# Performance work log

Measured on AMD Instinct MI355X. Metric: run time of the kernel, lower is better.

## Reference

```python
import jax, jax.numpy as jnp
import numpy as np

H = 8  # num_heads (init kwarg)

def setup_inputs() -> dict:
    key = jax.random.key(0)
    k1, k2, k3, k4 = jax.random.split(key, 4)
    B, S, E = 4, 2048, 512
    x = jax.random.normal(k1, (B, S, E), dtype=jnp.float32)
    # 'normal' keras initializer ~ N(0, 0.05)
    Wq = jax.random.normal(k2, (E, E), dtype=jnp.float32) * 0.05
    Wk = jax.random.normal(k3, (E, E), dtype=jnp.float32) * 0.05
    Wv = jax.random.normal(k4, (E, E), dtype=jnp.float32) * 0.05
    return {"x": x, "Wq": Wq, "Wk": Wk, "Wv": Wv}

def _split_heads(t):
    # [B,S,E] -> [H,B,S,E/H]; matches tf.stack(tf.split(t, H, axis=2))
    B, S, E = t.shape
    return t.reshape(B, S, H, E // H).transpose(2, 0, 1, 3)

def reference(x, Wq, Wk, Wv):
    B, S, E = x.shape
    q = _split_heads(jnp.einsum('bse,ef->bsf', x, Wq))  # [H,B,S,dh]
    k = _split_heads(jnp.einsum('bse,ef->bsf', x, Wk))
    v = _split_heads(jnp.einsum('bse,ef->bsf', x, Wv))
    # NOTE: original has NO 1/sqrt(d) scaling
    scores = jnp.einsum('hbqd,hbkd->hbqk', q, k)         # [H,B,S,S]
    attn = jax.nn.softmax(scores, axis=-1)
    effect = jnp.einsum('hbqk,hbkd->hbqd', attn, v)      # [H,B,S,dh]
    # tf.concat(tf.split(effect, H), axis=-1) + squeeze == merge heads on last dim
    out = effect.transpose(1, 2, 0, 3).reshape(B, S, E)  # [B,S,E]
    return (out, x)
```

## Files before the change

### kernel.cpp

```cpp
#include <hip/hip_runtime.h>

typedef _Float16 f16x8 __attribute__((ext_vector_type(8)));
typedef __fp16 h16x2 __attribute__((ext_vector_type(2)));
typedef float f32x4 __attribute__((ext_vector_type(4)));
typedef float f32x16 __attribute__((ext_vector_type(16)));

#define GF(r) ((((r)&3)) ^ (((r)>>2)&3))
#define LOG2E 1.44269504088896f

#define GLD16(gp, lp) __builtin_amdgcn_global_load_lds( \
    (const __attribute__((address_space(1))) void*)(gp), \
    (__attribute__((address_space(3))) void*)(lp), 16, 0, 0)

__global__ void cvt_all_kernel(const float4* __restrict__ x4, f16x8* __restrict__ xh,
                               float4* __restrict__ xc,
                               const float* __restrict__ Wq, const float* __restrict__ Wk,
                               const float* __restrict__ Wv, _Float16* __restrict__ wt) {
    const int blk = blockIdx.x;
    if (blk < 2048) {
        int i = blk * 256 + threadIdx.x;
        float4 a = x4[2 * i], b = x4[2 * i + 1];
        xc[2 * i] = a;
        xc[2 * i + 1] = b;
        f16x8 h;
        h[0] = (_Float16)a.x; h[1] = (_Float16)a.y; h[2] = (_Float16)a.z; h[3] = (_Float16)a.w;
        h[4] = (_Float16)b.x; h[5] = (_Float16)b.y; h[6] = (_Float16)b.z; h[7] = (_Float16)b.w;
        xh[i] = h;
    } else {
        int j = (blk - 2048) * 256 + threadIdx.x;
        int mat = j >> 18;
        int r = (j >> 9) & 511;
        int n = j & 511;
        const float* W = (mat == 0) ? Wq : ((mat == 1) ? Wk : Wv);
        float v = W[r * 512 + n];
        wt[(size_t)mat * 262144 + (size_t)n * 512 + r] = (_Float16)v;
    }
}

__global__ __launch_bounds__(256, 2) void gemm_qkv(
    const _Float16* __restrict__ xh, const _Float16* __restrict__ wt,
    _Float16* __restrict__ qh, _Float16* __restrict__ kh, _Float16* __restrict__ vt) {
    __shared__ __align__(16) char gsm[49152];
    const int mat = blockIdx.y;
    const _Float16* wp = wt + (size_t)mat * 262144;
    const int mtile = blockIdx.x >> 2, ntile = blockIdx.x & 3;
    const int tid = threadIdx.x, lane = tid & 63;
    const int g = lane >> 4, c = lane & 15;
    const int wid = tid >> 6, wm = wid >> 1, wn = wid & 1;

    f32x4 acc[4][4];
#pragma unroll
    for (int i = 0; i < 4; ++i)
#pragma unroll
        for (int j = 0; j < 4; ++j) acc[i][j] = (f32x4){0.f, 0.f, 0.f, 0.f};

    const int row0 = tid >> 2, p0 = tid & 3;

    auto GSTAGE = [&](int buf, int ks) {
        _Float16* la_ = (_Float16*)(gsm + buf * 16384);
        _Float16* lb_ = (_Float16*)(gsm + buf * 16384 + 8192);
        int r = row0, pp = p0 ^ GF(r);
        GLD16(xh + (size_t)(mtile * 128 + r) * 512 + ks * 32 + pp * 8, &la_[tid * 8]);
        GLD16(wp + (size_t)(ntile * 128 + r) * 512 + ks * 32 + pp * 8, &lb_[tid * 8]);
        r = 64 + row0; pp = p0 ^ GF(r);
        GLD16(xh + (size_t)(mtile * 128 + r) * 512 + ks * 32 + pp * 8, &la_[(256 + tid) * 8]);
        GLD16(wp + (size_t)(ntile * 128 + r) * 512 + ks * 32 + pp * 8, &lb_[(256 + tid) * 8]);
    };

    auto GTILE = [&](int ks) {
        const _Float16* la = (const _Float16*)(gsm + (ks % 3) * 16384);
        const _Float16* lb = (const _Float16*)(gsm + (ks % 3) * 16384 + 8192);
        f16x8 af[4], bf[4];
#pragma unroll
        for (int i = 0; i < 4; ++i) {
            int ra = wm * 64 + i * 16 + c;
            af[i] = *(const f16x8*)&la[ra * 32 + ((g ^ GF(ra)) * 8)];
            int rb = wn * 64 + i * 16 + c;
            bf[i] = *(const f16x8*)&lb[rb * 32 + ((g ^ GF(rb)) * 8)];
        }
        __builtin_amdgcn_s_setprio(1);
#pragma unroll
        for (int mi = 0; mi < 4; ++mi)
#pragma unroll
            for (int ni = 0; ni < 4; ++ni)
                acc[mi][ni] = __builtin_amdgcn_mfma_f32_16x16x32_f16(af[mi], bf[ni], acc[mi][ni], 0, 0, 0);
        __builtin_amdgcn_s_setprio(0);
    };

    GSTAGE(0, 0); GSTAGE(1, 1);
#pragma unroll 1
    for (int ks = 0; ks < 14; ++ks) {
        asm volatile("s_waitcnt vmcnt(4)" ::: "memory");
        __builtin_amdgcn_s_barrier();
        __builtin_amdgcn_sched_barrier(0);
        GSTAGE((ks + 2) % 3, ks + 2);
        GTILE(ks);
    }
    asm volatile("s_waitcnt vmcnt(4)" ::: "memory");
    __builtin_amdgcn_s_barrier();
    GTILE(14);
    asm volatile("s_waitcnt vmcnt(0)" ::: "memory");
    __builtin_amdgcn_s_barrier();
    GTILE(15);

#pragma unroll
    for (int mi = 0; mi < 4; ++mi)
#pragma unroll
        for (int ni = 0; ni < 4; ++ni)
#pragma unroll
            for (int r = 0; r < 4; ++r) {
                int m = mtile * 128 + wm * 64 + mi * 16 + g * 4 + r;
                int n = ntile * 128 + wn * 64 + ni * 16 + c;
                _Float16 hv = (_Float16)acc[mi][ni][r];
                if (mat == 0) {
                    qh[(size_t)m * 512 + n] = hv;
                } else if (mat == 1) {
                    kh[(size_t)m * 512 + n] = hv;
                } else {
                    int h = n >> 6, d = n & 63, bb = m >> 11, s = m & 2047;
                    vt[(((size_t)h * 4 + bb) * 64 + d) * 2048 + s] = hv;
                }
            }
}

__global__ __launch_bounds__(512, 4) void attn_kernel(
    const _Float16* __restrict__ qh, const _Float16* __restrict__ kh,
    const _Float16* __restrict__ vt, float* __restrict__ out) {
    __shared__ __align__(16) char smem[65536];

    const int bid = blockIdx.x;
    const int xcd = bid & 7, idx = bid >> 3;
    const int hb = xcd * 4 + (idx >> 4);
    const int qblk = idx & 15;
    const int h = hb >> 2, b = hb & 3;
    const int tid = threadIdx.x, lane = tid & 63, wid = tid >> 6;
    const int qg = wid & 3, half = wid >> 2;
    const int q = lane & 31, hi = lane >> 5;

    const int qrow0 = qblk * 128 + qg * 32;
    const _Float16* qp = qh + ((size_t)b * 2048 + qrow0) * 512 + h * 64;
    const _Float16* kp = kh + (size_t)b * 2048 * 512 + h * 64;
    const _Float16* vp = vt + (size_t)hb * 64 * 2048;

    const int srow = tid >> 3;
    const int ssw = (tid & 7) ^ ((srow ^ (srow >> 3)) & 7);

    auto STAGE = [&](int i) {
        char* base = smem + (i & 1) * 32768;
        GLD16(kp + ((size_t)(i * 64 + srow) * 512) + ssw * 8, (_Float16*)(base) + tid * 8);
        GLD16(vp + (size_t)srow * 2048 + i * 64 + ssw * 8, (_Float16*)(base + 8192) + tid * 8);
        GLD16(kp + ((size_t)((16 + i) * 64 + srow) * 512) + ssw * 8, (_Float16*)(base + 16384) + tid * 8);
        GLD16(vp + (size_t)srow * 2048 + (16 + i) * 64 + ssw * 8, (_Float16*)(base + 24576) + tid * 8);
    };

    f16x8 aQ[4];
#pragma unroll
    for (int kc = 0; kc < 4; ++kc)
        aQ[kc] = *(const f16x8*)(qp + (size_t)q * 512 + kc * 16 + hi * 8);

    float mrow = -1e30f, lrow = 0.f;
    f32x16 o0, o1;
#pragma unroll
    for (int i = 0; i < 16; ++i) { o0[i] = 0.f; o1[i] = 0.f; }

    const h16x2 ONE2 = {(__fp16)1.0f, (__fp16)1.0f};
    const int swr0 = (q ^ (q >> 3)) & 7;
    const int swr1 = ((32 + q) ^ ((32 + q) >> 3)) & 7;

    auto TILE = [&](int it) {
        const _Float16* kb = (const _Float16*)(smem + (it & 1) * 32768 + half * 16384);
        const _Float16* vb = kb + 4096;

        f32x16 s0, s1;
        __builtin_amdgcn_s_setprio(1);
        {
            f32x16 z0, z1;
#pragma unroll
            for (int i = 0; i < 16; ++i) { z0[i] = 0.f; z1[i] = 0.f; }
#pragma unroll
            for (int kc = 0; kc < 4; ++kc) {
                f16x8 ak0 = *(const f16x8*)&kb[q * 64 + (((2 * kc + hi) ^ swr0) * 8)];
                f16x8 ak1 = *(const f16x8*)&kb[(32 + q) * 64 + (((2 * kc + hi) ^ swr1) * 8)];
                z0 = __builtin_amdgcn_mfma_f32_32x32x16_f16(ak0, aQ[kc], z0, 0, 0, 0);
                z1 = __builtin_amdgcn_mfma_f32_32x32x16_f16(ak1, aQ[kc], z1, 0, 0, 0);
            }
            s0 = z0; s1 = z1;
        }
        __builtin_amdgcn_s_setprio(0);

        float pm;
        {
            float m0 = fmaxf(fmaxf(fmaxf(s0[0], s0[1]), s0[2]), s0[3]);
            float m1 = fmaxf(fmaxf(fmaxf(s0[4], s0[5]), s0[6]), s0[7]);
            float m2 = fmaxf(fmaxf(fmaxf(s0[8], s0[9]), s0[10]), s0[11]);
            float m3 = fmaxf(fmaxf(fmaxf(s0[12], s0[13]), s0[14]), s0[15]);
            float m4 = fmaxf(fmaxf(fmaxf(s1[0], s1[1]), s1[2]), s1[3]);
            float m5 = fmaxf(fmaxf(fmaxf(s1[4], s1[5]), s1[6]), s1[7]);
            float m6 = fmaxf(fmaxf(fmaxf(s1[8], s1[9]), s1[10]), s1[11]);
            float m7 = fmaxf(fmaxf(fmaxf(s1[12], s1[13]), s1[14]), s1[15]);
            float t0 = fmaxf(fmaxf(m0, m1), m2);
            float t1 = fmaxf(fmaxf(m3, m4), m5);
            float t2 = fmaxf(m6, m7);
            pm = fmaxf(fmaxf(t0, t1), t2);
        }
        pm = fmaxf(pm, __shfl_xor(pm, 32));
        if (__any(pm > mrow + 8.0f)) {
            const float nm = fmaxf(mrow, pm);
            const float e = __builtin_amdgcn_exp2f((mrow - nm) * LOG2E);
            mrow = nm;
            lrow *= e;
            o0 *= e;
            o1 *= e;
        }
        const float nm2 = mrow * LOG2E;

#pragma unroll
        for (int i = 0; i < 16; ++i)
            s0[i] = __builtin_amdgcn_exp2f(fmaf(s0[i], LOG2E, -nm2));
#pragma unroll
        for (int i = 0; i < 16; ++i)
            s1[i] = __builtin_amdgcn_exp2f(fmaf(s1[i], LOG2E, -nm2));

        f16x8 pf[4];
        float rsA = 0.f, rsB = 0.f;
#pragma unroll
        for (int kb2 = 0; kb2 < 2; ++kb2) {
            const f32x16& sv = kb2 ? s1 : s0;
            h16x2 p0 = __builtin_amdgcn_cvt_pkrtz(sv[0], sv[1]);
            h16x2 p1 = __builtin_amdgcn_cvt_pkrtz(sv[2], sv[3]);
            h16x2 p2 = __builtin_amdgcn_cvt_pkrtz(sv[4], sv[5]);
            h16x2 p3 = __builtin_amdgcn_cvt_pkrtz(sv[6], sv[7]);
            h16x2 p4 = __builtin_amdgcn_cvt_pkrtz(sv[8], sv[9]);
            h16x2 p5 = __builtin_amdgcn_cvt_pkrtz(sv[10], sv[11]);
            h16x2 p6 = __builtin_amdgcn_cvt_pkrtz(sv[12], sv[13]);
            h16x2 p7 = __builtin_amdgcn_cvt_pkrtz(sv[14], sv[15]);
            rsA = __builtin_amdgcn_fdot2(p0, ONE2, rsA, false);
            rsB = __builtin_amdgcn_fdot2(p1, ONE2, rsB, false);
            rsA = __builtin_amdgcn_fdot2(p2, ONE2, rsA, false);
            rsB = __builtin_amdgcn_fdot2(p3, ONE2, rsB, false);
            rsA = __builtin_amdgcn_fdot2(p4, ONE2, rsA, false);
            rsB = __builtin_amdgcn_fdot2(p5, ONE2, rsB, false);
            rsA = __builtin_amdgcn_fdot2(p6, ONE2, rsA, false);
            rsB = __builtin_amdgcn_fdot2(p7, ONE2, rsB, false);
            unsigned t0 = __builtin_bit_cast(unsigned, p0);
            unsigned t1 = __builtin_bit_cast(unsigned, p1);
            unsigned t2 = __builtin_bit_cast(unsigned, p2);
            unsigned t3 = __builtin_bit_cast(unsigned, p3);
            unsigned t4 = __builtin_bit_cast(unsigned, p4);
            unsigned t5 = __builtin_bit_cast(unsigned, p5);
            unsigned t6 = __builtin_bit_cast(unsigned, p6);
            unsigned t7 = __builtin_bit_cast(unsigned, p7);
            asm volatile("v_permlane32_swap_b32 %0, %1" : "+v"(t0), "+v"(t2));
            asm volatile("v_permlane32_swap_b32 %0, %1" : "+v"(t1), "+v"(t3));
            asm volatile("v_permlane32_swap_b32 %0, %1" : "+v"(t4), "+v"(t6));
            asm volatile("v_permlane32_swap_b32 %0, %1" : "+v"(t5), "+v"(t7));
            uint4 u0; u0.x = t0; u0.y = t1; u0.z = t2; u0.w = t3;
            uint4 u1; u1.x = t4; u1.y = t5; u1.z = t6; u1.w = t7;
            pf[2 * kb2 + 0] = __builtin_bit_cast(f16x8, u0);
            pf[2 * kb2 + 1] = __builtin_bit_cast(f16x8, u1);
        }
        lrow += rsA + rsB;

        __builtin_amdgcn_s_setprio(1);
        {
#pragma unroll
            for (int ck = 0; ck < 4; ++ck) {
                f16x8 av0 = *(const f16x8*)&vb[q * 64 + (((2 * ck + hi) ^ swr0) * 8)];
                f16x8 av1 = *(const f16x8*)&vb[(32 + q) * 64 + (((2 * ck + hi) ^ swr1) * 8)];
                o0 = __builtin_amdgcn_mfma_f32_32x32x16_f16(av0, pf[ck], o0, 0, 0, 0);
                o1 = __builtin_amdgcn_mfma_f32_32x32x16_f16(av1, pf[ck], o1, 0, 0, 0);
            }
        }
        __builtin_amdgcn_s_setprio(0);
    };

    STAGE(0);
#pragma unroll 1
    for (int it = 0; it < 16; ++it) {
        asm volatile("s_waitcnt vmcnt(0)" ::: "memory");
        __builtin_amdgcn_s_barrier();
        __builtin_amdgcn_sched_barrier(0);
        if (it < 15) STAGE(it + 1);
        TILE(it);
    }

    lrow += __shfl_xor(lrow, 32);
    __builtin_amdgcn_s_barrier();

    float* xg = (float*)smem + qg * 2112;
    if (half) {
#pragma unroll
        for (int i = 0; i < 16; ++i) {
            xg[i * 64 + lane] = o0[i];
            xg[(16 + i) * 64 + lane] = o1[i];
        }
        if (!hi) { xg[2048 + q] = mrow; xg[2080 + q] = lrow; }
    }
    __syncthreads();
    if (!half) {
        const float m_b = xg[2048 + q], l_b = xg[2080 + q];
        const float m = fmaxf(mrow, m_b);
        const float e_a = __builtin_amdgcn_exp2f((mrow - m) * LOG2E);
        const float e_b = __builtin_amdgcn_exp2f((m_b - m) * LOG2E);
        const float inv = 1.0f / (lrow * e_a + l_b * e_b);
        const float sa = e_a * inv, sb = e_b * inv;
#pragma unroll
        for (int i = 0; i < 16; ++i) {
            o0[i] = o0[i] * sa + xg[i * 64 + lane] * sb;
            o1[i] = o1[i] * sa + xg[(16 + i) * 64 + lane] * sb;
        }
        asm volatile("s_waitcnt lgkmcnt(0)" ::: "memory");
#pragma unroll
        for (int i = 0; i < 16; ++i) {
            int dr = (i & 3) + 8 * (i >> 2) + 4 * hi;
            xg[dr * 33 + q] = o0[i];
            xg[(32 + dr) * 33 + q] = o1[i];
        }
        __builtin_amdgcn_s_waitcnt(0);
        const int d0c = (lane & 15) * 4;
#pragma unroll
        for (int i2 = 0; i2 < 8; ++i2) {
            int qr = 4 * i2 + (lane >> 4);
            float4 v;
            v.x = xg[(d0c + 0) * 33 + qr];
            v.y = xg[(d0c + 1) * 33 + qr];
            v.z = xg[(d0c + 2) * 33 + qr];
            v.w = xg[(d0c + 3) * 33 + qr];
            *(float4*)(out + ((size_t)b * 2048 + qrow0 + qr) * 512 + h * 64 + d0c) = v;
        }
    }
}

extern "C" void kernel_launch(void* const* d_in, const int* in_sizes, int n_in,
                              void* d_out, int out_size, void* d_ws, size_t ws_size,
                              hipStream_t stream) {
    const float* x = (const float*)d_in[0];
    const float* Wq = (const float*)d_in[1];
    const float* Wk = (const float*)d_in[2];
    const float* Wv = (const float*)d_in[3];
    float* out = (float*)d_out;
    float* xcopy = out + 4194304;

    char* ws = (char*)d_ws;
    _Float16* xh = (_Float16*)ws;
    _Float16* wt = (_Float16*)(ws + (size_t)(10u << 20));
    _Float16* qh = (_Float16*)(ws + (size_t)(12u << 20));
    _Float16* kh = (_Float16*)(ws + (size_t)(20u << 20));
    _Float16* vt = (_Float16*)(ws + (size_t)(28u << 20));

    cvt_all_kernel<<<5120, 256, 0, stream>>>((const float4*)x, (f16x8*)xh, (float4*)xcopy,
                                             Wq, Wk, Wv, wt);
    gemm_qkv<<<dim3(256, 3), 256, 0, stream>>>(xh, wt, qh, kh, vt);
    attn_kernel<<<512, 512, 0, stream>>>(qh, kh, vt, out);
}
```

Baseline: 90.87 us.

## Stagger wave halves so QK^T of one half overlaps softmax/PV of other

Result: no change. 91.58 us (+0.8%).

```diff
diff --git a/kernel.cpp b/kernel.cpp
--- a/kernel.cpp
+++ b/kernel.cpp
@@ -167,27 +167,27 @@
     const int swr0 = (q ^ (q >> 3)) & 7;
     const int swr1 = ((32 + q) ^ ((32 + q) >> 3)) & 7;
 
-    auto TILE = [&](int it) {
-        const _Float16* kb = (const _Float16*)(smem + (it & 1) * 32768 + half * 16384);
-        const _Float16* vb = kb + 4096;
-
-        f32x16 s0, s1;
+    auto KPTR = [&](int t) {
+        return (const _Float16*)(smem + (t & 1) * 32768 + half * 16384);
+    };
+
+    auto QKT2 = [&](const _Float16* kb, f32x16& s0, f32x16& s1) {
+        f32x16 z0, z1;
+#pragma unroll
+        for (int i = 0; i < 16; ++i) { z0[i] = 0.f; z1[i] = 0.f; }
         __builtin_amdgcn_s_setprio(1);
-        {
-            f32x16 z0, z1;
-#pragma unroll
-            for (int i = 0; i < 16; ++i) { z0[i] = 0.f; z1[i] = 0.f; }
-#pragma unroll
-            for (int kc = 0; kc < 4; ++kc) {
-                f16x8 ak0 = *(const f16x8*)&kb[q * 64 + (((2 * kc + hi) ^ swr0) * 8)];
-                f16x8 ak1 = *(const f16x8*)&kb[(32 + q) * 64 + (((2 * kc + hi) ^ swr1) * 8)];
-                z0 = __builtin_amdgcn_mfma_f32_32x32x16_f16(ak0, aQ[kc], z0, 0, 0, 0);
-                z1 = __builtin_amdgcn_mfma_f32_32x32x16_f16(ak1, aQ[kc], z1, 0, 0, 0);
-            }
-            s0 = z0; s1 = z1;
+#pragma unroll
+        for (int kc = 0; kc < 4; ++kc) {
+            f16x8 ak0 = *(const f16x8*)&kb[q * 64 + (((2 * kc + hi) ^ swr0) * 8)];
+            f16x8 ak1 = *(const f16x8*)&kb[(32 + q) * 64 + (((2 * kc + hi) ^ swr1) * 8)];
+            z0 = __builtin_amdgcn_mfma_f32_32x32x16_f16(ak0, aQ[kc], z0, 0, 0, 0);
+            z1 = __builtin_amdgcn_mfma_f32_32x32x16_f16(ak1, aQ[kc], z1, 0, 0, 0);
         }
         __builtin_amdgcn_s_setprio(0);
-
+        s0 = z0; s1 = z1;
+    };
+
+    auto SMPV2 = [&](f32x16& s0, f32x16& s1, const _Float16* vb) {
         float pm;
         {
             float m0 = fmaxf(fmaxf(fmaxf(s0[0], s0[1]), s0[2]), s0[3]);
@@ -262,26 +262,44 @@
         lrow += rsA + rsB;
 
         __builtin_amdgcn_s_setprio(1);
-        {
-#pragma unroll
-            for (int ck = 0; ck < 4; ++ck) {
-                f16x8 av0 = *(const f16x8*)&vb[q * 64 + (((2 * ck + hi) ^ swr0) * 8)];
-                f16x8 av1 = *(const f16x8*)&vb[(32 + q) * 64 + (((2 * ck + hi) ^ swr1) * 8)];
-                o0 = __builtin_amdgcn_mfma_f32_32x32x16_f16(av0, pf[ck], o0, 0, 0, 0);
-                o1 = __builtin_amdgcn_mfma_f32_32x32x16_f16(av1, pf[ck], o1, 0, 0, 0);
-            }
+#pragma unroll
+        for (int ck = 0; ck < 4; ++ck) {
+            f16x8 av0 = *(const f16x8*)&vb[q * 64 + (((2 * ck + hi) ^ swr0) * 8)];
+            f16x8 av1 = *(const f16x8*)&vb[(32 + q) * 64 + (((2 * ck + hi) ^ swr1) * 8)];
+            o0 = __builtin_amdgcn_mfma_f32_32x32x16_f16(av0, pf[ck], o0, 0, 0, 0);
+            o1 = __builtin_amdgcn_mfma_f32_32x32x16_f16(av1, pf[ck], o1, 0, 0, 0);
         }
         __builtin_amdgcn_s_setprio(0);
     };
 
+#define WAITBAR() do { \
+    asm volatile("s_waitcnt vmcnt(0)" ::: "memory"); \
+    __builtin_amdgcn_s_barrier(); \
+    __builtin_amdgcn_sched_barrier(0); \
+} while (0)
+
+    f32x16 s0, s1;
     STAGE(0);
+    if (half == 0) {
 #pragma unroll 1
-    for (int it = 0; it < 16; ++it) {
-        asm volatile("s_waitcnt vmcnt(0)" ::: "memory");
-        __builtin_amdgcn_s_barrier();
-        __builtin_amdgcn_sched_barrier(0);
-        if (it < 15) STAGE(it + 1);
-        TILE(it);
+        for (int t = 0; t < 16; ++t) {
+            WAITBAR();
+            if (t < 15) STAGE(t + 1);
+            QKT2(KPTR(t), s0, s1);
+            SMPV2(s0, s1, KPTR(t) + 4096);
+        }
+    } else {
+        WAITBAR();
+        STAGE(1);
+        QKT2(KPTR(0), s0, s1);
+#pragma unroll 1
+        for (int t = 1; t < 16; ++t) {
+            SMPV2(s0, s1, KPTR(t - 1) + 4096);
+            WAITBAR();
+            if (t < 15) STAGE(t + 1);
+            QKT2(KPTR(t), s0, s1);
+        }
+        SMPV2(s0, s1, KPTR(15) + 4096);
     }
 
     lrow += __shfl_xor(lrow, 32);
@@ -329,6 +347,7 @@
             *(float4*)(out + ((size_t)b * 2048 + qrow0 + qr) * 512 + h * 64 + d0c) = v;
         }
     }
+#undef WAITBAR
 }
 
 extern "C" void kernel_launch(void* const* d_in, const int* in_sizes, int n_in,
```
